# Kernel optimization log

Hardware: AMD Instinct MI355X
Metric: run time of the kernel (lower is better)

The kernel has to match this reference:

```python
import jax, jax.numpy as jnp
import numpy as np

N = 50000
E = 800000

def _glorot(k, shape):
    lim = float(np.sqrt(6.0 / (shape[0] + shape[1])))
    return jax.random.uniform(k, shape, jnp.float32, -lim, lim)

def setup_inputs() -> dict:
    key = jax.random.key(0)
    ks = jax.random.split(key, 12)
    x = jax.random.normal(ks[0], (N, 58), jnp.float32)
    edge_index = jax.random.randint(ks[1], (2, E), 0, N, jnp.int32)
    neg_edge_index = jax.random.randint(ks[2], (2, E), 0, N, jnp.int32)
    return dict(
        x=x, edge_index=edge_index, neg_edge_index=neg_edge_index,
        W1_0=_glorot(ks[3], (58, 300)), W1_1=_glorot(ks[4], (58, 300)), b1=jnp.zeros((300,), jnp.float32),
        W2_0=_glorot(ks[5], (300, 100)), W2_1=_glorot(ks[6], (300, 100)), b2=jnp.zeros((100,), jnp.float32),
        W3_0=_glorot(ks[7], (100, 1)), W3_1=_glorot(ks[8], (100, 1)), b3=jnp.zeros((1,), jnp.float32),
        lin1_W=_glorot(ks[9], (100, 58)), lin1_b=jnp.zeros((100,), jnp.float32),
        lin2_W=_glorot(ks[10], (100, 58)), lin2_b=jnp.zeros((100,), jnp.float32),
        c1=jnp.full((1,), 0.5, jnp.float32), c2=jnp.full((1,), 0.5, jnp.float32),
    )

def _cheb(x, src, dst, norm, W0, W1, b):
    tx1 = jax.ops.segment_sum(x[src] * norm[:, None], dst, num_segments=x.shape[0])
    return x @ W0 + tx1 @ W1 + b

def reference(x, edge_index, neg_edge_index,
              W1_0, W1_1, b1, W2_0, W2_1, b2, W3_0, W3_1, b3,
              lin1_W, lin1_b, lin2_W, lin2_b, c1, c2):
    src, dst = edge_index[0], edge_index[1]
    deg = jax.ops.segment_sum(jnp.ones((E,), x.dtype), src, num_segments=N)
    dis = jnp.where(deg > 0, 1.0 / jnp.sqrt(jnp.where(deg > 0, deg, 1.0)), 0.0)
    norm = -(dis[src] * dis[dst])  # [E]
    h = jax.nn.relu(_cheb(x, src, dst, norm, W1_0, W1_1, b1))      # [N,300]
    x1 = jax.nn.relu(_cheb(h, src, dst, norm, W2_0, W2_1, b2))     # [N,100]
    xm = x1 + jax.nn.relu(x @ lin1_W.T + lin1_b)
    z = x1 + jax.nn.relu(x @ lin2_W.T + lin2_b)
    pos_score = jnp.sum(z[edge_index[0]] * z[edge_index[1]], axis=1)
    pos_loss = -jnp.mean(jnp.log(jax.nn.sigmoid(pos_score) + 1e-15))
    neg_score = jnp.sum(z[neg_edge_index[0]] * z[neg_edge_index[1]], axis=1)
    neg_loss = -jnp.mean(jnp.log(1.0 - jax.nn.sigmoid(neg_score) + 1e-15))
    r_loss = pos_loss + neg_loss
    out = _cheb(xm, src, dst, norm, W3_0, W3_1, b3)                # [N,1]
    return (out, r_loss, c1, c2)
```

## Files before the change

kernel.cpp:

```cpp
#include <hip/hip_runtime.h>
#include <math.h>

#define NN 50000
#define NE 800000
#define SB2 2048
#define LB 1024
#define CAP 64

using bf16x8 = __attribute__((ext_vector_type(8))) short;
using f32x4  = __attribute__((ext_vector_type(4))) float;
using f32x2  = __attribute__((ext_vector_type(2))) float;
using i32x8  = __attribute__((ext_vector_type(8))) int;

__device__ __forceinline__ float b2f(short s) {
    union { unsigned u; float f; } v;
    v.u = ((unsigned)(unsigned short)s) << 16;
    return v.f;
}
__device__ __forceinline__ unsigned short f2b(float f) {
    union { float f; unsigned u; } v;
    v.f = f;
    unsigned r = v.u + 0x7fffu + ((v.u >> 16) & 1u);
    return (unsigned short)(r >> 16);
}
__device__ __forceinline__ unsigned char f2e4m3(float f) {
    return (unsigned char)(__builtin_amdgcn_cvt_pk_fp8_f32(f, f, 0, false) & 0xff);
}
__device__ __forceinline__ void acc8(float* acc, uint2 u) {
    f32x2 p0 = __builtin_amdgcn_cvt_pk_f32_fp8(u.x, false);
    f32x2 p1 = __builtin_amdgcn_cvt_pk_f32_fp8(u.x, true);
    f32x2 p2 = __builtin_amdgcn_cvt_pk_f32_fp8(u.y, false);
    f32x2 p3 = __builtin_amdgcn_cvt_pk_f32_fp8(u.y, true);
    acc[0] += p0.x; acc[1] += p0.y;
    acc[2] += p1.x; acc[3] += p1.y;
    acc[4] += p2.x; acc[5] += p2.y;
    acc[6] += p3.x; acc[7] += p3.y;
}

__global__ void k_build(const int* __restrict__ ei, int* __restrict__ degs,
                        int* __restrict__ cnt, unsigned short* __restrict__ bkt16) {
    int e = blockIdx.x * 256 + threadIdx.x;
    if (e < NE) {
        int s = ei[e], d = ei[NE + e];
        atomicAdd(&degs[s], 1);
        int slot = atomicAdd(&cnt[d], 1);
        if (slot < CAP) bkt16[(d << 6) + slot] = (unsigned short)s;
    }
}

__global__ __launch_bounds__(256) void k_prep(const float* __restrict__ x,
                                              unsigned short* __restrict__ xcat,
                                              unsigned char* __restrict__ xf8,
                                              const int* __restrict__ degs,
                                              float* __restrict__ dis,
                                              const float* __restrict__ W1_0,
                                              const float* __restrict__ W1_1,
                                              const float* __restrict__ W2_0,
                                              const float* __restrict__ W2_1,
                                              const float* __restrict__ L1,
                                              const float* __restrict__ L2,
                                              unsigned short* __restrict__ Wt1f,
                                              unsigned short* __restrict__ Wt2f,
                                              unsigned short* __restrict__ Wtlf) {
    int b = blockIdx.x;
    if (b < 12500) {
        int t = b * 256 + threadIdx.x;
        int n = t >> 6, k = t & 63;
        float v = (k < 58) ? x[(size_t)n * 58 + k] : 0.0f;
        xcat[(size_t)n * 128 + k] = f2b(v);
        int dg = degs[n];
        float dv = dg > 0 ? 1.0f / sqrtf((float)dg) : 0.0f;
        xf8[(size_t)n * 64 + k] = f2e4m3(dv * v);
        return;
    }
    if (b < 12696) {
        int i = (b - 12500) * 256 + threadIdx.x;
        if (i < NN) {
            int dg = degs[i];
            dis[i] = dg > 0 ? 1.0f / sqrtf((float)dg) : 0.0f;
        }
        return;
    }
    int t = (b - 12696) * 256 + threadIdx.x;
    if (t < 40960) {
        int f = t >> 9, lane = (t >> 3) & 63, j = t & 7;
        int nt = f >> 2, s = f & 3;
        int ml = lane & 15, quad = lane >> 4;
        int k = s * 32 + quad * 8 + j;
        int col = nt * 16 + ml;
        float v = 0.0f;
        if (col < 300) {
            if (k < 58) v = W1_0[k * 300 + col];
            else if (k >= 64 && k < 122) v = W1_1[(k - 64) * 300 + col];
        }
        Wt1f[t] = f2b(v);
    } else if (t < 107520) {
        int u = t - 40960;
        int f = u >> 9, lane = (u >> 3) & 63, j = u & 7;
        int nt = f / 10, s = f - nt * 10;
        int ml = lane & 15, quad = lane >> 4;
        int k = s * 32 + quad * 8 + j;
        int col = nt * 16 + ml;
        float v = 0.0f;
        if (k < 300) {
            if (col < 100) v = W2_0[k * 100 + col];
            else if (col >= 104 && col < 204) v = W2_1[k * 100 + (col - 104)];
        }
        Wt2f[u] = f2b(v);
    } else if (t < 120832) {
        int u = t - 107520;
        int f = u >> 9, lane = (u >> 3) & 63, j = u & 7;
        int nt = f >> 1, s = f & 1;
        int ml = lane & 15, quad = lane >> 4;
        int k = s * 32 + quad * 8 + j;
        int col = nt * 16 + ml;
        float v = 0.0f;
        if (k < 58) {
            if (col < 100) v = L1[col * 58 + k];
            else if (col >= 104 && col < 204) v = L2[(col - 104) * 58 + k];
        }
        Wtlf[u] = f2b(v);
    }
}

__global__ __launch_bounds__(256) void k_gather58(const int* __restrict__ cnt,
                                                  const unsigned short* __restrict__ bkt16,
                                                  const float* __restrict__ dis,
                                                  const unsigned char* __restrict__ xf8,
                                                  unsigned short* __restrict__ xcat) {
    int t = blockIdx.x * 256 + threadIdx.x;
    int n = t >> 3, l = t & 7;
    if (n >= NN) return;
    int c = cnt[n]; if (c > CAP) c = CAP;
    float dn = dis[n];
    const unsigned short* bp = bkt16 + (n << 6);
    float acc[8] = {0, 0, 0, 0, 0, 0, 0, 0};
    for (int i = 0; i < c; i++) {
        unsigned src = bp[i];
        uint2 u = *(const uint2*)(xf8 + (size_t)src * 64 + l * 8);
        acc8(acc, u);
    }
    bf16x8 o;
#pragma unroll
    for (int j = 0; j < 8; j++) o[j] = (short)f2b(-dn * acc[j]);
    *(bf16x8*)(xcat + (size_t)n * 128 + 64 + l * 8) = o;
}

__global__ __launch_bounds__(256) void k_mm12(const unsigned short* __restrict__ xcat,
                                              const unsigned short* __restrict__ Wt1f,
                                              const float* __restrict__ b1,
                                              const unsigned short* __restrict__ Wt2f,
                                              const float* __restrict__ dis,
                                              float* __restrict__ hp,
                                              unsigned char* __restrict__ hwf8) {
    __shared__ __attribute__((aligned(16))) unsigned short hs[64 * 328];
    __shared__ __attribute__((aligned(16))) unsigned short bst[2][5120];
    int tid = threadIdx.x;
    int wave = tid >> 6, lane = tid & 63, ml = lane & 15, quad = lane >> 4;
    int row0 = blockIdx.x * 64;
    int rw = row0 + wave * 16;

    int ar = rw + ml; if (ar >= NN) ar = NN - 1;
    const bf16x8* Ap = (const bf16x8*)(xcat + (size_t)ar * 128 + quad * 8);
    bf16x8 a0 = Ap[0], a1 = Ap[4], a2 = Ap[8], a3 = Ap[12];
    float dv[4];
#pragma unroll
    for (int r = 0; r < 4; r++) {
        int row = rw + quad * 4 + r;
        dv[r] = dis[row < NN ? row : NN - 1];
    }

    ((bf16x8*)bst[0])[tid] = ((const bf16x8*)Wt1f)[tid];
    __syncthreads();

    for (int nt = 0; nt < 20; nt++) {
        if (nt + 1 < 20)
            ((bf16x8*)bst[(nt + 1) & 1])[tid] =
                ((const bf16x8*)(Wt1f + (size_t)(nt + 1) * 2048))[tid];
        const bf16x8* Bp = (const bf16x8*)bst[nt & 1];
        f32x4 acc = {0.f, 0.f, 0.f, 0.f};
        acc = __builtin_amdgcn_mfma_f32_16x16x32_bf16(a0, Bp[0 * 64 + lane], acc, 0, 0, 0);
        acc = __builtin_amdgcn_mfma_f32_16x16x32_bf16(a1, Bp[1 * 64 + lane], acc, 0, 0, 0);
        acc = __builtin_amdgcn_mfma_f32_16x16x32_bf16(a2, Bp[2 * 64 + lane], acc, 0, 0, 0);
        acc = __builtin_amdgcn_mfma_f32_16x16x32_bf16(a3, Bp[3 * 64 + lane], acc, 0, 0, 0);
        int col = nt * 16 + ml;
        float bias = (col < 300) ? b1[col] : 0.0f;
#pragma unroll
        for (int r = 0; r < 4; r++) {
            float v = acc[r] + bias;
            v = v > 0.0f ? v : 0.0f;
            if (col >= 300) v = 0.0f;
            hs[(wave * 16 + quad * 4 + r) * 328 + col] = f2b(v);
        }
        __syncthreads();
    }

    for (int i = tid; i < 640; i += 256)
        ((bf16x8*)bst[0])[i] = ((const bf16x8*)Wt2f)[i];
    bf16x8 A2[10];
#pragma unroll
    for (int s = 0; s < 10; s++)
        A2[s] = *(const bf16x8*)(hs + (wave * 16 + ml) * 328 + s * 32 + quad * 8);
    __syncthreads();

    for (int nt = 0; nt < 13; nt++) {
        if (nt + 1 < 13)
            for (int i = tid; i < 640; i += 256)
                ((bf16x8*)bst[(nt + 1) & 1])[i] =
                    ((const bf16x8*)(Wt2f + (size_t)(nt + 1) * 5120))[i];
        const bf16x8* Bp = (const bf16x8*)bst[nt & 1];
        f32x4 acc = {0.f, 0.f, 0.f, 0.f};
#pragma unroll
        for (int s = 0; s < 10; s++)
            acc = __builtin_amdgcn_mfma_f32_16x16x32_bf16(A2[s], Bp[s * 64 + lane], acc, 0, 0, 0);
        int j = nt * 16 + ml;
#pragma unroll
        for (int r = 0; r < 4; r++) {
            int row = rw + quad * 4 + r;
            if (row < NN) {
                if (j < 104) hp[(size_t)row * 104 + j] = acc[r];
                else hwf8[(size_t)row * 128 + (j - 104)] = f2e4m3(dv[r] * acc[r]);
            }
        }
        __syncthreads();
    }
}

__global__ __launch_bounds__(256) void k_mmlin2(const unsigned short* __restrict__ xcat,
                                                const unsigned short* __restrict__ Wtlf,
                                                const float* __restrict__ hp,
                                                const unsigned char* __restrict__ hwf8,
                                                const int* __restrict__ cnt,
                                                const unsigned short* __restrict__ bkt16,
                                                const float* __restrict__ dis,
                                                const float* __restrict__ b2,
                                                const float* __restrict__ l1b,
                                                const float* __restrict__ l2b,
                                                const float* __restrict__ W30,
                                                const float* __restrict__ W31,
                                                const float* __restrict__ b3,
                                                float* __restrict__ out,
                                                float* __restrict__ qbuf,
                                                unsigned char* __restrict__ zf8) {
    __shared__ float tx2s[64 * 104];
    int tid = threadIdx.x;
    int wave = tid >> 6, lane = tid & 63, ml = lane & 15, quad = lane >> 4;
    int row0 = blockIdx.x * 64;
    int rw = row0 + wave * 16;

    {
        int l = tid & 15, nd0 = tid >> 4;
        for (int sub = 0; sub < 4; sub++) {
            int nd = sub * 16 + nd0;
            int node = row0 + nd;
            if (node < NN && l < 13) {
                int c = cnt[node]; if (c > CAP) c = CAP;
                float dn = dis[node];
                const unsigned short* bp = bkt16 + (node << 6);
                float acc[8] = {0, 0, 0, 0, 0, 0, 0, 0};
                for (int i = 0; i < c; i++) {
                    unsigned src = bp[i];
                    uint2 u = *(const uint2*)(hwf8 + (size_t)src * 128 + l * 8);
                    acc8(acc, u);
                }
#pragma unroll
                for (int j = 0; j < 8; j++) tx2s[nd * 104 + l * 8 + j] = -dn * acc[j];
            }
        }
    }
    __syncthreads();

    int ar = rw + ml; if (ar >= NN) ar = NN - 1;
    const bf16x8* Ap = (const bf16x8*)(xcat + (size_t)ar * 128 + quad * 8);
    bf16x8 a0 = Ap[0], a1 = Ap[4];
    float p0[4] = {0, 0, 0, 0}, p1[4] = {0, 0, 0, 0};
    float b3v = b3[0];

    for (int nt = 0; nt < 13; nt++) {
        bf16x8 bw0 = *(const bf16x8*)(Wtlf + (size_t)((nt * 2 + 0) * 64 + lane) * 8);
        bf16x8 bw1 = *(const bf16x8*)(Wtlf + (size_t)((nt * 2 + 1) * 64 + lane) * 8);
        f32x4 acc = {0.f, 0.f, 0.f, 0.f};
        acc = __builtin_amdgcn_mfma_f32_16x16x32_bf16(a0, bw0, acc, 0, 0, 0);
        acc = __builtin_amdgcn_mfma_f32_16x16x32_bf16(a1, bw1, acc, 0, 0, 0);
        int j = nt * 16 + ml;
        int jj = (j < 104) ? j : j - 104;
        float bb = 0.0f, lb = 0.0f;
        if (jj < 100) {
            bb = b2[jj];
            lb = (j < 104) ? l1b[jj] : l2b[jj];
        }
        float w0 = (j < 100) ? W30[j] : 0.0f;
        float w1 = (j < 100) ? W31[j] : 0.0f;
#pragma unroll
        for (int r = 0; r < 4; r++) {
            int row = rw + quad * 4 + r;
            int rcl = row < NN ? row : NN - 1;
            float x1v = hp[(size_t)rcl * 104 + jj] + tx2s[(wave * 16 + quad * 4 + r) * 104 + jj] + bb;
            x1v = x1v > 0.0f ? x1v : 0.0f;
            float lv = acc[r] + lb;
            lv = lv > 0.0f ? lv : 0.0f;
            float o = x1v + lv;
            if (j < 104) {
                p0[r] += o * w0;
                p1[r] += o * w1;
            } else if (row < NN) {
                zf8[(size_t)row * 128 + (j - 104)] = f2e4m3(o);
            }
        }
    }
#pragma unroll
    for (int m = 1; m < 16; m <<= 1) {
#pragma unroll
        for (int r = 0; r < 4; r++) {
            p0[r] += __shfl_xor(p0[r], m, 64);
            p1[r] += __shfl_xor(p1[r], m, 64);
        }
    }
    if (ml == 0) {
#pragma unroll
        for (int r = 0; r < 4; r++) {
            int row = rw + quad * 4 + r;
            if (row < NN) {
                out[row] = p0[r] + b3v;
                qbuf[row] = dis[row] * p1[r];
            }
        }
    }
    for (int idx = tid; idx < 64 * 6; idx += 256) {
        int rr = row0 + idx / 6;
        if (rr < NN) *(unsigned*)(zf8 + (size_t)rr * 128 + 104 + (idx % 6) * 4) = 0u;
    }
}

__global__ __launch_bounds__(256) void k_score(const unsigned char* __restrict__ zf8,
                                               const int* __restrict__ ei,
                                               const int* __restrict__ nei,
                                               float* __restrict__ pbuf) {
    int lane = threadIdx.x & 63;
    int wid = (blockIdx.x * 256 + threadIdx.x) >> 6;
    int nw = SB2 * 4;
    int ml = lane & 15, quad = lane >> 4;
    int dr = ml - quad * 4;
    bool diag = (dr >= 0 && dr < 4);
    const int G = (2 * NE) / 16;
    for (int g = wid; g < G; g += nw) {
        int base = g * 16;
        int a, b;
        if (base < NE) {
            a = ei[base + ml];
            b = ei[NE + base + ml];
        } else {
            a = nei[base - NE + ml];
            b = nei[base + ml];
        }
        i32x8 av = *(const i32x8*)(zf8 + (size_t)a * 128 + quad * 32);
        i32x8 bv = *(const i32x8*)(zf8 + (size_t)b * 128 + quad * 32);
        f32x4 d = {0.f, 0.f, 0.f, 0.f};
        d = __builtin_amdgcn_mfma_scale_f32_16x16x128_f8f6f4(
                av, bv, d, 0, 0, 0, 0x7f7f7f7f, 0, 0x7f7f7f7f);
        if (diag) pbuf[base + ml] = d[dr];
    }
}

__global__ __launch_bounds__(256) void k_loss(const float* __restrict__ pbuf,
                                              double* __restrict__ red) {
    double acc = 0.0;
    for (int i = blockIdx.x * 256 + threadIdx.x; i < 2 * NE; i += LB * 256) {
        float p = pbuf[i];
        float sg = 1.0f / (1.0f + expf(-p));
        float term = (i < NE) ? logf(sg + 1e-15f) : logf(1.0f - sg + 1e-15f);
        acc += (double)term;
    }
    __shared__ double sred[256];
    sred[threadIdx.x] = acc;
    __syncthreads();
    for (int s = 128; s; s >>= 1) {
        if (threadIdx.x < s) sred[threadIdx.x] += sred[threadIdx.x + s];
        __syncthreads();
    }
    if (threadIdx.x == 0) red[blockIdx.x] = sred[0];
}

__global__ __launch_bounds__(256) void k_final_g1(const double* __restrict__ red,
                                                  const float* __restrict__ c1,
                                                  const float* __restrict__ c2,
                                                  const int* __restrict__ cnt,
                                                  const unsigned short* __restrict__ bkt16,
                                                  const float* __restrict__ dis,
                                                  const float* __restrict__ qbuf,
                                                  float* __restrict__ out) {
    if (blockIdx.x == 0) {
        double a = 0.0;
        for (int i = threadIdx.x; i < LB; i += 256) a += red[i];
        __shared__ double sred[256];
        sred[threadIdx.x] = a;
        __syncthreads();
        for (int st = 128; st; st >>= 1) {
            if (threadIdx.x < st) sred[threadIdx.x] += sred[threadIdx.x + st];
            __syncthreads();
        }
        if (threadIdx.x == 0) {
            out[NN] = (float)(-sred[0] / (double)NE);
            out[NN + 1] = c1[0];
            out[NN + 2] = c2[0];
        }
        return;
    }
    int n = (blockIdx.x - 1) * 256 + threadIdx.x;
    if (n >= NN) return;
    int c = cnt[n]; if (c > CAP) c = CAP;
    const unsigned short* bp = bkt16 + (n << 6);
    float acc = 0.0f;
    for (int i = 0; i < c; i++) acc += qbuf[bp[i]];
    out[n] += -dis[n] * acc;
}

extern "C" void kernel_launch(void* const* d_in, const int* in_sizes, int n_in,
                              void* d_out, int out_size, void* d_ws, size_t ws_size,
                              hipStream_t stream) {
    const float* x    = (const float*)d_in[0];
    const int*   ei   = (const int*)d_in[1];
    const int*   nei  = (const int*)d_in[2];
    const float* W1_0 = (const float*)d_in[3];
    const float* W1_1 = (const float*)d_in[4];
    const float* b1   = (const float*)d_in[5];
    const float* W2_0 = (const float*)d_in[6];
    const float* W2_1 = (const float*)d_in[7];
    const float* b2   = (const float*)d_in[8];
    const float* W3_0 = (const float*)d_in[9];
    const float* W3_1 = (const float*)d_in[10];
    const float* b3   = (const float*)d_in[11];
    const float* l1W  = (const float*)d_in[12];
    const float* l1b  = (const float*)d_in[13];
    const float* l2W  = (const float*)d_in[14];
    const float* l2b  = (const float*)d_in[15];
    const float* c1   = (const float*)d_in[16];
    const float* c2   = (const float*)d_in[17];
    float* out = (float*)d_out;
    float* w = (float*)d_ws;

    unsigned short* bkt16  = (unsigned short*)w;
    int*            degs   = (int*)(w + 1600000);
    int*            cnt    = (int*)(w + 1650000);
    float*          dis    = w + 1700000;
    float*          qbuf   = w + 1750000;
    double*         red    = (double*)(w + 1800000);
    float*          pbuf   = w + 1802048;
    unsigned short* xcat   = (unsigned short*)(w + 3402048);
    unsigned short* Wt1f   = (unsigned short*)(w + 6602048);
    unsigned short* Wt2f   = (unsigned short*)(w + 6622528);
    unsigned short* Wtlf   = (unsigned short*)(w + 6655808);
    float*          hp     = w + 6662464;
    unsigned char*  hwf8   = (unsigned char*)(w + 11862464);
    unsigned char*  zf8    = (unsigned char*)(w + 13462464);
    unsigned char*  xf8    = (unsigned char*)(w + 15062464);

    hipMemsetAsync(degs, 0, 100000 * sizeof(int), stream);

    k_build<<<(NE + 255) / 256, 256, 0, stream>>>(ei, degs, cnt, bkt16);
    k_prep<<<13168, 256, 0, stream>>>(x, xcat, xf8, degs, dis,
                                      W1_0, W1_1, W2_0, W2_1, l1W, l2W,
                                      Wt1f, Wt2f, Wtlf);

    k_gather58<<<(NN * 8 + 255) / 256, 256, 0, stream>>>(cnt, bkt16, dis, xf8, xcat);
    k_mm12<<<(NN + 63) / 64, 256, 0, stream>>>(xcat, Wt1f, b1, Wt2f, dis, hp, hwf8);

    k_mmlin2<<<(NN + 63) / 64, 256, 0, stream>>>(xcat, Wtlf, hp, hwf8, cnt, bkt16, dis,
                                                 b2, l1b, l2b, W3_0, W3_1, b3,
                                                 out, qbuf, zf8);

    k_score<<<SB2, 256, 0, stream>>>(zf8, ei, nei, pbuf);
    k_loss<<<LB, 256, 0, stream>>>(pbuf, red);
    k_final_g1<<<1 + (NN + 255) / 256, 256, 0, stream>>>(red, c1, c2, cnt, bkt16, dis, qbuf, out);
}
```

Before: 429.7 us.

## Split layer-2 neighbor gather out of fused matmul kernel into its own kernel

Moves the fp8 neighbor aggregation for layer 2 out of the mmlin kernel into a separate k_gather100 kernel. That kernel writes tx2 to a global fp32 buffer, and the matmul kernel then reads it instead of shared memory. The intent is to let the irregular gather run at full occupancy without 26KB of shared memory, and to let the MFMA kernel drop its barrier and shared-memory pressure. The cost is an extra launch plus a round trip of about 20MB through global memory for tx2.

```diff
diff --git a/kernel.cpp b/kernel.cpp
--- a/kernel.cpp
+++ b/kernel.cpp
@@ -226,12 +226,33 @@
     }
 }
 
-__global__ __launch_bounds__(256) void k_mmlin2(const unsigned short* __restrict__ xcat,
+__global__ __launch_bounds__(256) void k_gather100(const int* __restrict__ cnt,
+                                                   const unsigned short* __restrict__ bkt16,
+                                                   const float* __restrict__ dis,
+                                                   const unsigned char* __restrict__ hwf8,
+                                                   float* __restrict__ tx2) {
+    int t = blockIdx.x * 256 + threadIdx.x;
+    int n = t >> 4, l = t & 15;
+    if (n >= NN || l >= 13) return;
+    int c = cnt[n]; if (c > CAP) c = CAP;
+    float dn = dis[n];
+    const unsigned short* bp = bkt16 + (n << 6);
+    float acc[8] = {0, 0, 0, 0, 0, 0, 0, 0};
+    for (int i = 0; i < c; i++) {
+        unsigned src = bp[i];
+        uint2 u = *(const uint2*)(hwf8 + (size_t)src * 128 + l * 8);
+        acc8(acc, u);
+    }
+    f32x4 o0 = {-dn * acc[0], -dn * acc[1], -dn * acc[2], -dn * acc[3]};
+    f32x4 o1 = {-dn * acc[4], -dn * acc[5], -dn * acc[6], -dn * acc[7]};
+    *(f32x4*)(tx2 + (size_t)n * 104 + l * 8) = o0;
+    *(f32x4*)(tx2 + (size_t)n * 104 + l * 8 + 4) = o1;
+}
+
+__global__ __launch_bounds__(256) void k_mmlin3(const unsigned short* __restrict__ xcat,
                                                 const unsigned short* __restrict__ Wtlf,
                                                 const float* __restrict__ hp,
-                                                const unsigned char* __restrict__ hwf8,
-                                                const int* __restrict__ cnt,
-                                                const unsigned short* __restrict__ bkt16,
+                                                const float* __restrict__ tx2,
                                                 const float* __restrict__ dis,
                                                 const float* __restrict__ b2,
                                                 const float* __restrict__ l1b,
@@ -242,33 +263,11 @@
                                                 float* __restrict__ out,
                                                 float* __restrict__ qbuf,
                                                 unsigned char* __restrict__ zf8) {
-    __shared__ float tx2s[64 * 104];
     int tid = threadIdx.x;
     int wave = tid >> 6, lane = tid & 63, ml = lane & 15, quad = lane >> 4;
     int row0 = blockIdx.x * 64;
     int rw = row0 + wave * 16;
-
-    {
-        int l = tid & 15, nd0 = tid >> 4;
-        for (int sub = 0; sub < 4; sub++) {
-            int nd = sub * 16 + nd0;
-            int node = row0 + nd;
-            if (node < NN && l < 13) {
-                int c = cnt[node]; if (c > CAP) c = CAP;
-                float dn = dis[node];
-                const unsigned short* bp = bkt16 + (node << 6);
-                float acc[8] = {0, 0, 0, 0, 0, 0, 0, 0};
-                for (int i = 0; i < c; i++) {
-                    unsigned src = bp[i];
-                    uint2 u = *(const uint2*)(hwf8 + (size_t)src * 128 + l * 8);
-                    acc8(acc, u);
-                }
-#pragma unroll
-                for (int j = 0; j < 8; j++) tx2s[nd * 104 + l * 8 + j] = -dn * acc[j];
-            }
-        }
-    }
-    __syncthreads();
+    if (rw >= NN) return;
 
     int ar = rw + ml; if (ar >= NN) ar = NN - 1;
     const bf16x8* Ap = (const bf16x8*)(xcat + (size_t)ar * 128 + quad * 8);
@@ -295,7 +294,7 @@
         for (int r = 0; r < 4; r++) {
             int row = rw + quad * 4 + r;
             int rcl = row < NN ? row : NN - 1;
-            float x1v = hp[(size_t)rcl * 104 + jj] + tx2s[(wave * 16 + quad * 4 + r) * 104 + jj] + bb;
+            float x1v = hp[(size_t)rcl * 104 + jj] + tx2[(size_t)rcl * 104 + jj] + bb;
             x1v = x1v > 0.0f ? x1v : 0.0f;
             float lv = acc[r] + lb;
             lv = lv > 0.0f ? lv : 0.0f;
@@ -326,8 +325,8 @@
             }
         }
     }
-    for (int idx = tid; idx < 64 * 6; idx += 256) {
-        int rr = row0 + idx / 6;
+    for (int idx = lane; idx < 16 * 6; idx += 64) {
+        int rr = rw + idx / 6;
         if (rr < NN) *(unsigned*)(zf8 + (size_t)rr * 128 + 104 + (idx % 6) * 4) = 0u;
     }
 }
@@ -454,6 +453,7 @@
     unsigned char*  hwf8   = (unsigned char*)(w + 11862464);
     unsigned char*  zf8    = (unsigned char*)(w + 13462464);
     unsigned char*  xf8    = (unsigned char*)(w + 15062464);
+    float*          tx2    = w + 15862464;
 
     hipMemsetAsync(degs, 0, 100000 * sizeof(int), stream);
 
@@ -465,7 +465,8 @@
     k_gather58<<<(NN * 8 + 255) / 256, 256, 0, stream>>>(cnt, bkt16, dis, xf8, xcat);
     k_mm12<<<(NN + 63) / 64, 256, 0, stream>>>(xcat, Wt1f, b1, Wt2f, dis, hp, hwf8);
 
-    k_mmlin2<<<(NN + 63) / 64, 256, 0, stream>>>(xcat, Wtlf, hp, hwf8, cnt, bkt16, dis,
+    k_gather100<<<NN * 16 / 256, 256, 0, stream>>>(cnt, bkt16, dis, hwf8, tx2);
+    k_mmlin3<<<(NN + 63) / 64, 256, 0, stream>>>(xcat, Wtlf, hp, tx2, dis,
                                                  b2, l1b, l2b, W3_0, W3_1, b3,
                                                  out, qbuf, zf8);
 
```

Result: faster. 369.5 us (-14.0%).
